# Performance work log

Hardware: AMD Instinct MI355X
Metric: run time of the kernel (lower is better)

Reference implementation:

```python
import jax, jax.numpy as jnp
import numpy as np

N_ATOMS = 128
BATCH = 512


def _build_buffers(n):
    # Segments: all non-adjacent bond pairs (i,i+1,j,j+1), j >= i+2, j+1 <= n-1.
    segs = np.array([(i, i + 1, j, j + 1)
                     for i in range(n - 3)
                     for j in range(i + 2, n - 1)], dtype=np.int32)  # (S,4)

    def pidx(a, b):  # linear index of pair (a,b), a<b, in row-major triu(offset=1) order
        return a * n - a * (a + 1) // 2 + (b - a - 1)

    # Each writhe value scatters into its 4 incident residue pairs.
    # Pairs (0,1) [triu idx 0] and (n-2,n-1) [last triu idx] are never incident,
    # so ranks among interior pairs are (triu idx - 1); they are re-inserted by pad.
    inc = []
    for (i, _, j, _) in segs:
        for (a, b) in ((i, j), (i, j + 1), (i + 1, j), (i + 1, j + 1)):
            inc.append(pidx(a, b) - 1)
    indices = np.array(inc, dtype=np.int32)  # (4*S,)

    # Sort permutation placing [upper-triu values, lower-triu values] into
    # row-major order of all off-diagonal (r,c) entries, keyed by r*n + c.
    iu = np.stack(np.triu_indices(n, 1))  # (2, P) row-major
    vals = np.concatenate([iu[0] * n + iu[1], iu[1] * n + iu[0]])
    sort = np.argsort(vals).astype(np.int32)  # (n^2 - n,)
    return segs, indices, sort


def setup_inputs() -> dict:
    key = jax.random.key(0)
    xyz = jax.random.normal(key, (BATCH, N_ATOMS, 3), dtype=jnp.float32)
    segs, indices, sort = _build_buffers(N_ATOMS)
    return {
        "xyz": xyz,
        "segments": jnp.asarray(segs),
        "indices": jnp.asarray(indices),
        "sort": jnp.asarray(sort),
    }


def _divnorm(x):
    return x / jnp.linalg.norm(x, axis=-1, keepdims=True)


def _writhe(xyz, segments):
    # xyz: (B,N,3); segments: (S,4) -> writhe per segment pair, (B,S)
    B, S = xyz.shape[0], segments.shape[0]
    p = xyz[:, segments]  # (B,S,4,3) gathered endpoints [s1a,s1b,s2a,s2b]
    # d[k] = normalize(p_{2+j} - p_i), k = 2*i + j  (the 4 inter-segment directions)
    d = _divnorm((p[:, :, None, 2:, :] - p[:, :, :2, None, :]).reshape(B, S, 4, 3))
    axial = jnp.cross(p[:, :, 3] - p[:, :, 2], p[:, :, 1] - p[:, :, 0])  # (B,S,3)
    signs = jnp.sign(jnp.sum(axial * d[:, :, 0], -1))  # (B,S)
    # 4 face normals of the spherical quadrilateral, then Gauss-Bonnet angle sum
    nrm = _divnorm(jnp.cross(d[:, :, jnp.array([0, 1, 3, 2])],
                             d[:, :, jnp.array([1, 3, 2, 0])]))  # (B,S,4,3)
    cosang = jnp.clip(jnp.sum(nrm * nrm[:, :, jnp.array([1, 2, 3, 0])], -1), -1.0, 1.0)
    omega = jnp.arcsin(cosang).sum(-1)  # (B,S)
    return omega * signs / (2.0 * jnp.pi)


def _laplacian(wr, indices, sort, n):
    # wr: (B,S); scatter-add each writhe into its 4 incident residue pairs,
    # pad back the two untouched pairs, symmetrize, and sort into row-major
    # off-diagonal order -> (B, n^2 - n)
    M = (n * n - n) // 2 - 2
    triu = jnp.zeros((wr.shape[0], M), wr.dtype).at[:, indices].add(
        jnp.repeat(wr, 4, axis=1))
    padded = jnp.pad(triu, ((0, 0), (1, 1)))
    return jnp.concatenate([padded, padded], axis=1)[:, sort]


def reference(xyz, segments, indices, sort):
    xyz = xyz.reshape(-1, N_ATOMS, 3)
    wr = _writhe(xyz, segments)
    return _laplacian(wr, indices, sort, N_ATOMS)
```

## Files before the change

### kernel.cpp

```cpp
#include <hip/hip_runtime.h>
#include <math.h>

#define NATOMS    128
#define NSEG      7875
#define NSEG_PAD  8192
#define NPAIR     8128
#define OUT_PER_B 16256
#define BLOCK     512

typedef float v2f __attribute__((ext_vector_type(2)));
__device__ __forceinline__ v2f mk2(float a, float b) { v2f r; r.x = a; r.y = b; return r; }

struct P3 { v2f x, y, z; };
__device__ __forceinline__ P3 psub(P3 a, P3 b) { return {a.x - b.x, a.y - b.y, a.z - b.z}; }
__device__ __forceinline__ P3 pcross(P3 a, P3 b) {
    return {a.y * b.z - a.z * b.y, a.z * b.x - a.x * b.z, a.x * b.y - a.y * b.x};
}
__device__ __forceinline__ v2f pdot(P3 a, P3 b) { return a.x * b.x + a.y * b.y + a.z * b.z; }
__device__ __forceinline__ v2f prsq(v2f q) {
    v2f r; r.x = __builtin_amdgcn_rsqf(q.x); r.y = __builtin_amdgcn_rsqf(q.y); return r;
}
__device__ __forceinline__ v2f pclip1(v2f x) {
    return __builtin_elementwise_min(__builtin_elementwise_max(x, mk2(-1.f, -1.f)),
                                     mk2(1.f, 1.f));
}

__device__ __forceinline__ v2f fast_asin2(v2f x) {
    v2f a = __builtin_elementwise_abs(x);
    v2f p = mk2(-0.0187293f, -0.0187293f);
    p = p * a + mk2( 0.0742610f,  0.0742610f);
    p = p * a + mk2(-0.2121144f, -0.2121144f);
    p = p * a + mk2( 1.5707288f,  1.5707288f);
    v2f om = mk2(1.0f, 1.0f) - a;
    v2f sq; sq.x = __builtin_amdgcn_sqrtf(om.x); sq.y = __builtin_amdgcn_sqrtf(om.y);
    v2f r = mk2(1.57079632679f, 1.57079632679f) - sq * p;
    return __builtin_elementwise_copysign(r, x);
}

__device__ __forceinline__ int seg_row_base(int i) { return 125 * i - (__umul24(i, i - 1) >> 1); }

__device__ __forceinline__ v2f seg_writhe_pair(unsigned pa, unsigned pb,
                                               const float* sx, const float* sy,
                                               const float* sz) {
    int jA = (int)(pa & 127u), iA = (int)(pa >> 7);
    int jB = (int)(pb & 127u), iB = (int)(pb >> 7);

    P3 p0 = {mk2(sx[iA],     sx[iB]),     mk2(sy[iA],     sy[iB]),     mk2(sz[iA],     sz[iB])};
    P3 p1 = {mk2(sx[iA + 1], sx[iB + 1]), mk2(sy[iA + 1], sy[iB + 1]), mk2(sz[iA + 1], sz[iB + 1])};
    P3 p2 = {mk2(sx[jA],     sx[jB]),     mk2(sy[jA],     sy[jB]),     mk2(sz[jA],     sz[jB])};
    P3 p3 = {mk2(sx[jA + 1], sx[jB + 1]), mk2(sy[jA + 1], sy[jB + 1]), mk2(sz[jA + 1], sz[jB + 1])};

    P3 u0 = psub(p2, p0);
    P3 u1 = psub(p3, p0);
    P3 u2 = psub(p2, p1);
    P3 u3 = psub(p3, p1);

    P3 n0 = pcross(u0, u1);
    P3 n1 = pcross(u1, u3);
    P3 n2 = pcross(u3, u2);
    P3 n3 = pcross(u2, u0);

    v2f q0 = pdot(n0, n0);
    v2f q1 = pdot(n1, n1);
    v2f q2 = pdot(n2, n2);
    v2f q3 = pdot(n3, n3);

    v2f c0 = pclip1(pdot(n0, n1) * prsq(q0 * q1));
    v2f c1 = pclip1(pdot(n1, n2) * prsq(q1 * q2));
    v2f c2 = pclip1(pdot(n2, n3) * prsq(q2 * q3));
    v2f c3 = pclip1(pdot(n3, n0) * prsq(q3 * q0));

    v2f sd = pdot(n2, u0);
    v2f omega = fast_asin2(c0) + fast_asin2(c1) + fast_asin2(c2) + fast_asin2(c3);

    v2f sgn;
    sgn.x = (sd.x > 0.f) ? -1.f : ((sd.x < 0.f) ? 1.f : 0.f);
    sgn.y = (sd.y > 0.f) ? -1.f : ((sd.y < 0.f) ? 1.f : 0.f);

    return omega * sgn * mk2(0.15915494309189535f, 0.15915494309189535f);
}

__global__ __launch_bounds__(BLOCK, 4) void writhe_fused(
    const float* __restrict__ xyz,
    float*       __restrict__ out)
{
    __shared__ float sx[NATOMS], sy[NATOMS], sz[NATOMS];
    __shared__ float swr[NSEG_PAD];
    __shared__ unsigned short sidx[NSEG_PAD];

    const int b = blockIdx.x;
    const int t = threadIdx.x;

    if (t < 3 * NATOMS) {
        float v = xyz[(size_t)b * (3 * NATOMS) + t];
        int a = t / 3, c = t - 3 * a;
        if (c == 0) sx[a] = v; else if (c == 1) sy[a] = v; else sz[a] = v;
    }

    {
        int s = t * 16;
        if (s < NSEG) {
            int i = (int)((251.0f - __builtin_amdgcn_sqrtf(63001.0f - 8.0f * (float)s)) * 0.5f);
            i = max(i, 0);
            i += (seg_row_base(i + 1) <= s);
            i += (seg_row_base(i + 1) <= s);
            i -= (seg_row_base(i) > s);
            i -= (seg_row_base(i) > s);
            int j = s - seg_row_base(i) + i + 2;
            #pragma unroll
            for (int k = 0; k < 16; ++k) {
                if (s < NSEG) sidx[s] = (unsigned short)((i << 7) | j);
                ++s; ++j;
                if (j > 126) { ++i; j = i + 2; }
            }
        }
        if (t < NSEG_PAD - NSEG) sidx[NSEG + t] = (unsigned short)((124 << 7) | 126);
    }
    __syncthreads();

    #pragma unroll
    for (int g = 0; g < 4; ++g) {
        const int sA = g * 2048 + t;
        v2f w1 = seg_writhe_pair(sidx[sA],        sidx[sA + 512],  sx, sy, sz);
        v2f w2 = seg_writhe_pair(sidx[sA + 1024], sidx[sA + 1536], sx, sy, sz);
        swr[sA]        = w1.x;
        swr[sA + 512]  = w1.y;
        swr[sA + 1024] = w2.x;
        swr[sA + 1536] = w2.y;
    }
    __syncthreads();

    float* ob = out + (size_t)b * OUT_PER_B;
    for (int kq = t; kq < OUT_PER_B / 4; kq += BLOCK) {
        const int k0 = kq << 2;
        float acc[4];
        #pragma unroll
        for (int q = 0; q < 4; ++q) {
            const int k = k0 + q;
            const int r = (int)(((unsigned)k * 132105u) >> 24);
            int c = k - r * 127;
            c += (c >= r);
            const int a  = min(r, c);
            const int bb = max(r, c);

            const int am1 = a - 1;
            const int s00 = 125 * am1 - ((am1 * (am1 - 1)) >> 1) + bb - a - 2;
            const int s10 = s00 + 125 - a;

            const bool v00 = (a >= 1) && (a <= 125) && (bb >= a + 2);
            const bool v01 = (a >= 1) && (a <= 125) && (bb <= 126);
            const bool v10 = (a <= 124) && (bb >= a + 3);
            const bool v11 = (a <= 124) && (bb <= 126) && (bb >= a + 2);

            const int c00 = min(max(s00,     0), NSEG - 1);
            const int c01 = min(max(s00 + 1, 0), NSEG - 1);
            const int c10 = min(max(s10,     0), NSEG - 1);
            const int c11 = min(max(s10 + 1, 0), NSEG - 1);

            acc[q] = (v00 ? swr[c00] : 0.0f) + (v01 ? swr[c01] : 0.0f)
                   + (v10 ? swr[c10] : 0.0f) + (v11 ? swr[c11] : 0.0f);
        }
        float4 res; res.x = acc[0]; res.y = acc[1]; res.z = acc[2]; res.w = acc[3];
        *reinterpret_cast<float4*>(ob + k0) = res;
    }
}

extern "C" void kernel_launch(void* const* d_in, const int* in_sizes, int n_in,
                              void* d_out, int out_size, void* d_ws, size_t ws_size,
                              hipStream_t stream) {
    const float* xyz = (const float*)d_in[0];
    float*       out = (float*)d_out;

    int B = in_sizes[0] / (NATOMS * 3);
    writhe_fused<<<B, BLOCK, 0, stream>>>(xyz, out);
}
```

Baseline: 91.58 us.

## Reuse cross products across consecutive segments via per-thread chains

Each thread now handles four consecutive segments per lane, so the cross product, norm and direction vectors shared between segment j and j+1 are carried forward instead of recomputed. This also removes the index table in shared memory. Coordinates move into an interleaved float4 array so each atom is read with one load. Output writes switch to nontemporal stores. The risks are extra register pressure from the carried state, and branches at row boundaries where a chain has to be reseeded.

```diff
diff --git a/kernel.cpp b/kernel.cpp
--- a/kernel.cpp
+++ b/kernel.cpp
@@ -7,8 +7,10 @@
 #define NPAIR     8128
 #define OUT_PER_B 16256
 #define BLOCK     512
+#define NCHUNK    2048
 
 typedef float v2f __attribute__((ext_vector_type(2)));
+typedef float v4f __attribute__((ext_vector_type(4)));
 __device__ __forceinline__ v2f mk2(float a, float b) { v2f r; r.x = a; r.y = b; return r; }
 
 struct P3 { v2f x, y, z; };
@@ -39,44 +41,100 @@
 
 __device__ __forceinline__ int seg_row_base(int i) { return 125 * i - (__umul24(i, i - 1) >> 1); }
 
-__device__ __forceinline__ v2f seg_writhe_pair(unsigned pa, unsigned pb,
-                                               const float* sx, const float* sy,
-                                               const float* sz) {
-    int jA = (int)(pa & 127u), iA = (int)(pa >> 7);
-    int jB = (int)(pb & 127u), iB = (int)(pb >> 7);
-
-    P3 p0 = {mk2(sx[iA],     sx[iB]),     mk2(sy[iA],     sy[iB]),     mk2(sz[iA],     sz[iB])};
-    P3 p1 = {mk2(sx[iA + 1], sx[iB + 1]), mk2(sy[iA + 1], sy[iB + 1]), mk2(sz[iA + 1], sz[iB + 1])};
-    P3 p2 = {mk2(sx[jA],     sx[jB]),     mk2(sy[jA],     sy[jB]),     mk2(sz[jA],     sz[jB])};
-    P3 p3 = {mk2(sx[jA + 1], sx[jB + 1]), mk2(sy[jA + 1], sy[jB + 1]), mk2(sz[jA + 1], sz[jB + 1])};
-
-    P3 u0 = psub(p2, p0);
-    P3 u1 = psub(p3, p0);
-    P3 u2 = psub(p2, p1);
-    P3 u3 = psub(p3, p1);
-
-    P3 n0 = pcross(u0, u1);
+__device__ __forceinline__ void seed_ij(int s, int &i, int &j) {
+    i = (int)((251.0f - __builtin_amdgcn_sqrtf(63001.0f - 8.0f * (float)s)) * 0.5f);
+    i = max(i, 0);
+    i += (seg_row_base(i + 1) <= s);
+    i += (seg_row_base(i + 1) <= s);
+    i -= (seg_row_base(i) > s);
+    i -= (seg_row_base(i) > s);
+    j = s - seg_row_base(i) + i + 2;
+}
+
+__device__ __forceinline__ bool adv(int &i, int &j) {
+    ++j;
+    bool c = (j > 126);
+    int i2 = i + 1;
+    bool over = (i2 > 124);
+    int ni = over ? 124 : i2;
+    int nj = over ? 126 : (i2 + 2);
+    i = c ? ni : i;
+    j = c ? nj : j;
+    return c;
+}
+
+__device__ __forceinline__ P3 pack3(const float4 &a, const float4 &b) {
+    return { mk2(a.x, b.x), mk2(a.y, b.y), mk2(a.z, b.z) };
+}
+__device__ __forceinline__ v2f sel2(v2f o, v2f n, bool cA, bool cB) {
+    v2f r; r.x = cA ? n.x : o.x; r.y = cB ? n.y : o.y; return r;
+}
+__device__ __forceinline__ P3 sel3(P3 o, P3 n, bool cA, bool cB) {
+    return { sel2(o.x, n.x, cA, cB), sel2(o.y, n.y, cA, cB), sel2(o.z, n.z, cA, cB) };
+}
+
+struct Chain {
+    P3 p0, p1;
+    P3 u1p, u3p, n1p;
+    v2f q1p;
+    int iA, jA, iB, jB;
+};
+
+__device__ __forceinline__ void chain_init(Chain &ch, int sA, int sB, const float4 *sp4) {
+    seed_ij(min(sA, NSEG - 1), ch.iA, ch.jA);
+    seed_ij(min(sB, NSEG - 1), ch.iB, ch.jB);
+    float4 a0 = sp4[ch.iA], a1 = sp4[ch.iA + 1], a2 = sp4[ch.jA];
+    float4 b0 = sp4[ch.iB], b1 = sp4[ch.iB + 1], b2 = sp4[ch.jB];
+    ch.p0 = pack3(a0, b0); ch.p1 = pack3(a1, b1);
+    P3 p2 = pack3(a2, b2);
+    ch.u1p = psub(p2, ch.p0);
+    ch.u3p = psub(p2, ch.p1);
+    ch.n1p = pcross(ch.u1p, ch.u3p);
+    ch.q1p = pdot(ch.n1p, ch.n1p);
+}
+
+__device__ __forceinline__ void chain_advance(Chain &ch, const float4 *sp4) {
+    bool cA = adv(ch.iA, ch.jA);
+    bool cB = adv(ch.iB, ch.jB);
+    if (cA || cB) {
+        float4 a0 = sp4[ch.iA], a1 = sp4[ch.iA + 1], a2 = sp4[ch.jA];
+        float4 b0 = sp4[ch.iB], b1 = sp4[ch.iB + 1], b2 = sp4[ch.jB];
+        P3 np0 = pack3(a0, b0), np1 = pack3(a1, b1), np2 = pack3(a2, b2);
+        P3 nu1 = psub(np2, np0), nu3 = psub(np2, np1);
+        P3 nn1 = pcross(nu1, nu3);
+        v2f nq1 = pdot(nn1, nn1);
+        ch.p0  = sel3(ch.p0,  np0, cA, cB);
+        ch.p1  = sel3(ch.p1,  np1, cA, cB);
+        ch.u1p = sel3(ch.u1p, nu1, cA, cB);
+        ch.u3p = sel3(ch.u3p, nu3, cA, cB);
+        ch.n1p = sel3(ch.n1p, nn1, cA, cB);
+        ch.q1p = sel2(ch.q1p, nq1, cA, cB);
+    }
+}
+
+__device__ __forceinline__ v2f chain_step(Chain &ch, const float4 *sp4) {
+    float4 a3 = sp4[ch.jA + 1];
+    float4 b3 = sp4[ch.jB + 1];
+    P3 p3 = pack3(a3, b3);
+    P3 u1 = psub(p3, ch.p0);
+    P3 u3 = psub(p3, ch.p1);
+    P3 n0 = pcross(ch.u1p, u1);
     P3 n1 = pcross(u1, u3);
-    P3 n2 = pcross(u3, u2);
-    P3 n3 = pcross(u2, u0);
-
-    v2f q0 = pdot(n0, n0);
-    v2f q1 = pdot(n1, n1);
-    v2f q2 = pdot(n2, n2);
-    v2f q3 = pdot(n3, n3);
-
-    v2f c0 = pclip1(pdot(n0, n1) * prsq(q0 * q1));
-    v2f c1 = pclip1(pdot(n1, n2) * prsq(q1 * q2));
-    v2f c2 = pclip1(pdot(n2, n3) * prsq(q2 * q3));
-    v2f c3 = pclip1(pdot(n3, n0) * prsq(q3 * q0));
-
-    v2f sd = pdot(n2, u0);
+    P3 n2 = pcross(u3, ch.u3p);
+    v2f q0 = pdot(n0, n0), q1 = pdot(n1, n1), q2 = pdot(n2, n2);
+    v2f d01 = pdot(n0, n1), d12 = pdot(n1, n2);
+    v2f d23 = pdot(n2, ch.n1p);
+    v2f d30 = pdot(ch.n1p, n0);
+    v2f sd  = pdot(n2, ch.u1p);
+    v2f c0 = pclip1(d01 * prsq(q0 * q1));
+    v2f c1 = pclip1(d12 * prsq(q1 * q2));
+    v2f c2 = pclip1((-d23) * prsq(q2 * ch.q1p));
+    v2f c3 = pclip1((-d30) * prsq(ch.q1p * q0));
     v2f omega = fast_asin2(c0) + fast_asin2(c1) + fast_asin2(c2) + fast_asin2(c3);
-
     v2f sgn;
     sgn.x = (sd.x > 0.f) ? -1.f : ((sd.x < 0.f) ? 1.f : 0.f);
     sgn.y = (sd.y > 0.f) ? -1.f : ((sd.y < 0.f) ? 1.f : 0.f);
-
+    ch.u1p = u1; ch.u3p = u3; ch.n1p = n1; ch.q1p = q1;
     return omega * sgn * mk2(0.15915494309189535f, 0.15915494309189535f);
 }
 
@@ -84,9 +142,8 @@
     const float* __restrict__ xyz,
     float*       __restrict__ out)
 {
-    __shared__ float sx[NATOMS], sy[NATOMS], sz[NATOMS];
-    __shared__ float swr[NSEG_PAD];
-    __shared__ unsigned short sidx[NSEG_PAD];
+    __shared__ float4 sp4[NATOMS];
+    __shared__ float  swr[NSEG_PAD];
 
     const int b = blockIdx.x;
     const int t = threadIdx.x;
@@ -94,39 +151,32 @@
     if (t < 3 * NATOMS) {
         float v = xyz[(size_t)b * (3 * NATOMS) + t];
         int a = t / 3, c = t - 3 * a;
-        if (c == 0) sx[a] = v; else if (c == 1) sy[a] = v; else sz[a] = v;
-    }
+        ((float*)&sp4[a])[c] = v;
+    }
+    __syncthreads();
 
     {
-        int s = t * 16;
-        if (s < NSEG) {
-            int i = (int)((251.0f - __builtin_amdgcn_sqrtf(63001.0f - 8.0f * (float)s)) * 0.5f);
-            i = max(i, 0);
-            i += (seg_row_base(i + 1) <= s);
-            i += (seg_row_base(i + 1) <= s);
-            i -= (seg_row_base(i) > s);
-            i -= (seg_row_base(i) > s);
-            int j = s - seg_row_base(i) + i + 2;
-            #pragma unroll
-            for (int k = 0; k < 16; ++k) {
-                if (s < NSEG) sidx[s] = (unsigned short)((i << 7) | j);
-                ++s; ++j;
-                if (j > 126) { ++i; j = i + 2; }
-            }
+        Chain c0, c1;
+        chain_init(c0, 4 * t,          4 * (t + 512),  sp4);
+        chain_init(c1, 4 * (t + 1024), 4 * (t + 1536), sp4);
+
+        v2f wA[4], wB[4];
+        #pragma unroll
+        for (int k = 0; k < 4; ++k) {
+            if (k) { chain_advance(c0, sp4); chain_advance(c1, sp4); }
+            wA[k] = chain_step(c0, sp4);
+            wB[k] = chain_step(c1, sp4);
         }
-        if (t < NSEG_PAD - NSEG) sidx[NSEG + t] = (unsigned short)((124 << 7) | 126);
-    }
-    __syncthreads();
-
-    #pragma unroll
-    for (int g = 0; g < 4; ++g) {
-        const int sA = g * 2048 + t;
-        v2f w1 = seg_writhe_pair(sidx[sA],        sidx[sA + 512],  sx, sy, sz);
-        v2f w2 = seg_writhe_pair(sidx[sA + 1024], sidx[sA + 1536], sx, sy, sz);
-        swr[sA]        = w1.x;
-        swr[sA + 512]  = w1.y;
-        swr[sA + 1024] = w2.x;
-        swr[sA + 1536] = w2.y;
+
+        v4f r;
+        r.x = wA[0].x; r.y = wA[1].x; r.z = wA[2].x; r.w = wA[3].x;
+        *reinterpret_cast<v4f*>(swr + 4 * t)          = r;
+        r.x = wA[0].y; r.y = wA[1].y; r.z = wA[2].y; r.w = wA[3].y;
+        *reinterpret_cast<v4f*>(swr + 4 * t + 2048)   = r;
+        r.x = wB[0].x; r.y = wB[1].x; r.z = wB[2].x; r.w = wB[3].x;
+        *reinterpret_cast<v4f*>(swr + 4 * t + 4096)   = r;
+        r.x = wB[0].y; r.y = wB[1].y; r.z = wB[2].y; r.w = wB[3].y;
+        *reinterpret_cast<v4f*>(swr + 4 * t + 6144)   = r;
     }
     __syncthreads();
 
@@ -160,8 +210,8 @@
             acc[q] = (v00 ? swr[c00] : 0.0f) + (v01 ? swr[c01] : 0.0f)
                    + (v10 ? swr[c10] : 0.0f) + (v11 ? swr[c11] : 0.0f);
         }
-        float4 res; res.x = acc[0]; res.y = acc[1]; res.z = acc[2]; res.w = acc[3];
-        *reinterpret_cast<float4*>(ob + k0) = res;
+        v4f res; res.x = acc[0]; res.y = acc[1]; res.z = acc[2]; res.w = acc[3];
+        __builtin_nontemporal_store(res, reinterpret_cast<v4f*>(ob + k0));
     }
 }
 
```

Result: slower. 238.6 us (+160.5%).
